# Performance work log

Measured on AMD Instinct MI355X. Metric: run time of the kernel, lower is better.

The kernel has to match this reference:

```python
import jax, jax.numpy as jnp
import numpy as np

NB_SAMPLES = 16
GAMMA = 0.04       # also the noise_intensity passed to randomArgmax
ALPHA = 1.0
EPS = 1e-10


def setup_inputs() -> dict:
    key = jax.random.key(0)
    k1, k2, k3 = jax.random.split(key, 3)
    B, H, W, K = 8, 128, 128, 32
    zbuf = jax.random.normal(k1, (B, H, W, K), dtype=jnp.float32)
    prob_map = jax.random.uniform(k2, (B, H, W, K), dtype=jnp.float32)
    mask = jnp.ones((B, H, W, K), dtype=jnp.float32)
    zfar = jnp.ones((1,), dtype=jnp.float32)
    znear = jnp.zeros((1,), dtype=jnp.float32)
    # gaussian noise normally drawn inside randomArgmax.forward; made explicit for determinism
    noise = jax.random.normal(k3, (NB_SAMPLES, B, H, W, K + 1), dtype=jnp.float32)
    return {"zbuf": zbuf, "zfar": zfar, "znear": znear,
            "prob_map": prob_map, "mask": mask, "noise": noise}


def _random_argmax(z, noise, sigma):
    # z: [B,H,W,C]; noise: [S,B,H,W,C]
    C = z.shape[-1]
    z_pert = z[None] + sigma * noise                       # [S,B,H,W,C]
    idx = jnp.argmax(z_pert, axis=-1)                      # first-max, matches torch.max
    weights = jax.nn.one_hot(idx, C, dtype=z.dtype)        # [S,B,H,W,C]
    return weights.mean(axis=0)                            # [B,H,W,C]


def reference(zbuf, zfar, znear, prob_map, mask, noise):
    # inverse depth, masked
    z_inv = (zfar - zbuf) / (zfar - znear) * mask          # [B,H,W,K]
    z_inv_max = jnp.maximum(jnp.max(z_inv, axis=-1, keepdims=True), EPS)
    z_map = GAMMA / ALPHA * jnp.log(1e-12 + prob_map) + z_inv - z_inv_max
    bg = EPS - z_inv_max                                   # background channel [B,H,W,1]
    z_map = jnp.concatenate([z_map, bg], axis=-1)          # [B,H,W,K+1]
    return _random_argmax(z_map, noise, GAMMA)
```

## Files before the change

kernel.cpp:

```cpp
#include <hip/hip_runtime.h>


#define NPIX   (8 * 128 * 128)
#define KCH    32
#define CCH    33
#define SAMP   16
#define TPB    256
#define TILE   (TPB * CCH)

__global__ __launch_bounds__(TPB)
void gauss_agg_kernel(const float* __restrict__ zbuf,
                      const float* __restrict__ zfar_p,
                      const float* __restrict__ znear_p,
                      const float* __restrict__ prob,
                      const float* __restrict__ mask,
                      const float* __restrict__ noise,
                      float* __restrict__ out)
{
#pragma clang fp contract(off)
    __shared__ float lds[TILE];
    const int tid = threadIdx.x;
    const int p0  = blockIdx.x * TPB;
    const size_t p = (size_t)p0 + tid;

    const float zfar  = zfar_p[0];
    const float znear = znear_p[0];
    const float denom = zfar - znear;

    float zb[KCH], pm[KCH], mk[KCH];
    {
        const float4* zb4 = reinterpret_cast<const float4*>(zbuf + p * KCH);
        const float4* pm4 = reinterpret_cast<const float4*>(prob + p * KCH);
        const float4* mk4 = reinterpret_cast<const float4*>(mask + p * KCH);
        #pragma unroll
        for (int i = 0; i < KCH / 4; ++i) {
            float4 a = zb4[i], b = pm4[i], c = mk4[i];
            zb[4*i+0] = a.x; zb[4*i+1] = a.y; zb[4*i+2] = a.z; zb[4*i+3] = a.w;
            pm[4*i+0] = b.x; pm[4*i+1] = b.y; pm[4*i+2] = b.z; pm[4*i+3] = b.w;
            mk[4*i+0] = c.x; mk[4*i+1] = c.y; mk[4*i+2] = c.z; mk[4*i+3] = c.w;
        }
    }

    float z_inv[KCH];
    float zmax = 1e-10f;
    #pragma unroll
    for (int k = 0; k < KCH; ++k) {
        float zi = ((zfar - zb[k]) / denom) * mk[k];
        z_inv[k] = zi;
        zmax = fmaxf(zmax, zi);
    }

    float z_map[CCH];
    #pragma unroll
    for (int k = 0; k < KCH; ++k) {
        float lg = logf(1e-12f + pm[k]);
        z_map[k] = ((0.04f * lg) + z_inv[k]) - zmax;
    }
    z_map[KCH] = 1e-10f - zmax;

    int acc[CCH];
    #pragma unroll
    for (int c = 0; c < CCH; ++c) acc[c] = 0;

    for (int s = 0; s < SAMP; ++s) {
        __syncthreads();
        {
            const float4* g4 = reinterpret_cast<const float4*>(
                noise + ((size_t)s * NPIX + p0) * CCH);
            float4* l4 = reinterpret_cast<float4*>(lds);
            for (int i = tid; i < TILE / 4; i += TPB) l4[i] = g4[i];
        }
        __syncthreads();

        const int base = tid * CCH;
        float best = z_map[0] + (0.04f * lds[base + 0]);
        int bi = 0;
        #pragma unroll
        for (int c = 1; c < CCH; ++c) {
            float v = z_map[c] + (0.04f * lds[base + c]);
            if (v > best) { best = v; bi = c; }
        }
        #pragma unroll
        for (int c = 0; c < CCH; ++c) acc[c] += (bi == c) ? 1 : 0;
    }

    __syncthreads();
    {
        const int base = tid * CCH;
        #pragma unroll
        for (int c = 0; c < CCH; ++c)
            lds[base + c] = (float)acc[c] * 0.0625f;
    }
    __syncthreads();
    {
        const float4* l4 = reinterpret_cast<const float4*>(lds);
        float4* o4 = reinterpret_cast<float4*>(out + (size_t)p0 * CCH);
        for (int i = tid; i < TILE / 4; i += TPB) o4[i] = l4[i];
    }
}

extern "C" void kernel_launch(void* const* d_in, const int* in_sizes, int n_in,
                              void* d_out, int out_size, void* d_ws, size_t ws_size,
                              hipStream_t stream)
{
    const float* zbuf  = (const float*)d_in[0];
    const float* zfar  = (const float*)d_in[1];
    const float* znear = (const float*)d_in[2];
    const float* prob  = (const float*)d_in[3];
    const float* mask  = (const float*)d_in[4];
    const float* noise = (const float*)d_in[5];
    float* out = (float*)d_out;

    dim3 grid(NPIX / TPB), block(TPB);
    gauss_agg_kernel<<<grid, block, 0, stream>>>(zbuf, zfar, znear, prob, mask,
                                                 noise, out);
}
```

Baseline: 428.6 us.

## Double-buffer noise tiles in LDS using async global_load_lds prefetch

Replaces the register-mediated global-to-LDS copy of each sample's noise tile with direct global_load_lds transfers. The LDS tile is double-buffered so the next sample is prefetched while the current one is processed, and the first tile is issued before the per-pixel preprocessing. This is meant to hide global memory latency and drop one barrier per sample. In exchange it doubles LDS use to about 67 KB per block, which may reduce occupancy, and it relies on __syncthreads to cover completion of the async LDS writes (vmcnt waits), which the compiler may not guarantee.

```diff
diff --git a/kernel.cpp b/kernel.cpp
--- a/kernel.cpp
+++ b/kernel.cpp
@@ -7,6 +7,25 @@
 #define SAMP   16
 #define TPB    256
 #define TILE   (TPB * CCH)
+
+#define GLL16(gp, lp)                                                     \
+    __builtin_amdgcn_global_load_lds(                                     \
+        (const __attribute__((address_space(1))) void*)(gp),              \
+        (__attribute__((address_space(3))) void*)(lp), 16, 0, 0)
+
+__device__ __forceinline__ void stage_tile(const float* __restrict__ gsrc,
+                                           float* ldst, int tid)
+{
+    #pragma unroll
+    for (int j = 0; j < (TILE / 4) / TPB; ++j) {
+        const int i = tid + j * TPB;
+        GLL16(gsrc + 4 * i, ldst + 4 * i);
+    }
+    if (tid < (TILE / 4) - ((TILE / 4) / TPB) * TPB) {
+        const int i = tid + ((TILE / 4) / TPB) * TPB;
+        GLL16(gsrc + 4 * i, ldst + 4 * i);
+    }
+}
 
 __global__ __launch_bounds__(TPB)
 void gauss_agg_kernel(const float* __restrict__ zbuf,
@@ -18,10 +37,12 @@
                       float* __restrict__ out)
 {
 #pragma clang fp contract(off)
-    __shared__ float lds[TILE];
+    __shared__ float lds[2 * TILE];
     const int tid = threadIdx.x;
     const int p0  = blockIdx.x * TPB;
     const size_t p = (size_t)p0 + tid;
+
+    stage_tile(noise + ((size_t)0 * NPIX + p0) * CCH, lds, tid);
 
     const float zfar  = zfar_p[0];
     const float znear = znear_p[0];
@@ -62,29 +83,28 @@
     #pragma unroll
     for (int c = 0; c < CCH; ++c) acc[c] = 0;
 
+    __syncthreads();
+
     for (int s = 0; s < SAMP; ++s) {
-        __syncthreads();
-        {
-            const float4* g4 = reinterpret_cast<const float4*>(
-                noise + ((size_t)s * NPIX + p0) * CCH);
-            float4* l4 = reinterpret_cast<float4*>(lds);
-            for (int i = tid; i < TILE / 4; i += TPB) l4[i] = g4[i];
-        }
-        __syncthreads();
+        if (s + 1 < SAMP)
+            stage_tile(noise + ((size_t)(s + 1) * NPIX + p0) * CCH,
+                       lds + ((s + 1) & 1) * TILE, tid);
 
+        const float* cur = lds + (s & 1) * TILE;
         const int base = tid * CCH;
-        float best = z_map[0] + (0.04f * lds[base + 0]);
+        float best = z_map[0] + (0.04f * cur[base + 0]);
         int bi = 0;
         #pragma unroll
         for (int c = 1; c < CCH; ++c) {
-            float v = z_map[c] + (0.04f * lds[base + c]);
+            float v = z_map[c] + (0.04f * cur[base + c]);
             if (v > best) { best = v; bi = c; }
         }
         #pragma unroll
         for (int c = 0; c < CCH; ++c) acc[c] += (bi == c) ? 1 : 0;
+
+        __syncthreads();
     }
 
-    __syncthreads();
     {
         const int base = tid * CCH;
         #pragma unroll
```

Measured after the change: 408.6 us. -4.7%, faster.
